# Kernel tuning notes

Measured on AMD Instinct MI355X. Metric: run time of the kernel, lower is better.

## Reference

```python
import jax, jax.numpy as jnp
import numpy as np

B, S, E, H, U = 2048, 64, 512, 512, 512

def setup_inputs() -> dict:
    key = jax.random.key(0)
    ks = jax.random.split(key, 6)
    s = lambda d: 1.0 / np.sqrt(d)
    return {
        "features": jax.random.normal(ks[0], (B, S, E), jnp.float32),
        "hidden": jax.random.normal(ks[1], (B, H), jnp.float32),
        "W1": jax.random.normal(ks[2], (E, U), jnp.float32) * s(E),
        "b1": jnp.zeros((U,), jnp.float32),
        "W2": jax.random.normal(ks[3], (H, U), jnp.float32) * s(H),
        "b2": jnp.zeros((U,), jnp.float32),
        "Wv": jax.random.normal(ks[4], (U, 1), jnp.float32) * s(U),
        "bv": jnp.zeros((1,), jnp.float32),
    }

def reference(features, hidden, W1, b1, W2, b2, Wv, bv):
    # Bahdanau additive attention (dropout at inference = identity).
    h1 = jnp.einsum('bse,eu->bsu', features, W1) + b1          # [B,S,U]
    h2 = hidden @ W2 + b2                                       # [B,U]
    scores = jnp.tanh(h1 + h2[:, None, :]) @ Wv + bv            # [B,S,1]
    weights = jax.nn.softmax(scores, axis=1)                    # softmax over seq
    context = jnp.sum(weights * features, axis=1)               # [B,E]
    return context
```

## Files before the change

kernel.cpp:

```cpp
#include <hip/hip_runtime.h>

typedef _Float16 f16x8 __attribute__((ext_vector_type(8)));
typedef unsigned short u16x4 __attribute__((ext_vector_type(4)));
typedef float f32x4 __attribute__((ext_vector_type(4)));

#define VMWAIT(N) asm volatile("s_waitcnt vmcnt(" #N ")" ::: "memory")
#define LGKM0()   asm volatile("s_waitcnt lgkmcnt(0)" ::: "memory")
#define FENCE()   asm volatile("" ::: "memory")
#define RBAR()    do { FENCE(); __builtin_amdgcn_s_barrier(); FENCE(); } while (0)

__device__ __forceinline__ u16x4 cvt4(float4 v) {
    u16x4 h;
    h[0] = __builtin_bit_cast(unsigned short, (_Float16)v.x);
    h[1] = __builtin_bit_cast(unsigned short, (_Float16)v.y);
    h[2] = __builtin_bit_cast(unsigned short, (_Float16)v.z);
    h[3] = __builtin_bit_cast(unsigned short, (_Float16)v.w);
    return h;
}

__global__ void convert_w_kernel(const float* __restrict__ w1,
                                 const float* __restrict__ w2,
                                 unsigned short* __restrict__ w1img,
                                 unsigned short* __restrict__ w2img) {
    int u = blockIdx.x;
    int k = threadIdx.x + blockIdx.y * 256;
    size_t idx = (size_t)(k >> 5) * 16384 + (size_t)u * 32 + (k & 31);
    _Float16 h1 = (_Float16)w1[(size_t)k * 512 + u];
    _Float16 h2 = (_Float16)w2[(size_t)k * 512 + u];
    w1img[idx] = __builtin_bit_cast(unsigned short, h1);
    w2img[idx] = __builtin_bit_cast(unsigned short, h2);
}

__device__ __forceinline__ void stage_a64(const float* __restrict__ src,
                                          char* As, int tid) {
    const int row = tid >> 2, q = tid & 3;
    const float* p = src + (size_t)row * 512 + q * 4;
    const int sw2 = ((row >> 1) & 3) << 4;
    char* wb = As + row * 64;
    float4 va[4], vb[4];
#define AISS(V, G) { _Pragma("unroll") \
    for (int j_ = 0; j_ < 4; ++j_) V[j_] = *(const float4*)(p + ((G) * 4 + j_) * 16); }
#define APRC(V, G) { _Pragma("unroll") \
    for (int j_ = 0; j_ < 4; ++j_) { \
        const int i_ = (G) * 4 + j_; \
        *(u16x4*)(wb + (i_ >> 1) * 4096 + ((q * 8 + (i_ & 1) * 32) ^ sw2)) = cvt4(V[j_]); } }
    AISS(va, 0); AISS(vb, 1);
    VMWAIT(4); APRC(va, 0); AISS(va, 2);
    VMWAIT(4); APRC(vb, 1); AISS(vb, 3);
    VMWAIT(4); APRC(va, 2); AISS(va, 4);
    VMWAIT(4); APRC(vb, 3); AISS(vb, 5);
    VMWAIT(4); APRC(va, 4); AISS(va, 6);
    VMWAIT(4); APRC(vb, 5); AISS(vb, 7);
    VMWAIT(4); APRC(va, 6);
    VMWAIT(0); APRC(vb, 7);
#undef AISS
#undef APRC
}

__device__ __forceinline__ void chunk_gemm(const char* __restrict__ bcol,
                                           const char* As, const int* aoff,
                                           f32x4 acc[4][4]) {
    f16x8 brA[4], brB[4], afA[4], afB[4];
    #pragma unroll
    for (int i = 0; i < 4; ++i)
        #pragma unroll
        for (int j = 0; j < 4; ++j) acc[i][j] = (f32x4){0.f, 0.f, 0.f, 0.f};
    #pragma unroll
    for (int j = 0; j < 4; ++j) brA[j] = *(const f16x8*)(bcol + j * 1024);
    #pragma unroll
    for (int j = 0; j < 4; ++j) brB[j] = *(const f16x8*)(bcol + 32768 + j * 1024);
    #pragma unroll
    for (int i = 0; i < 4; ++i) afA[i] = *(const f16x8*)(As + aoff[i]);
    #pragma unroll
    for (int tt = 0; tt < 8; ++tt) {
        const int t0 = 2 * tt, t1 = t0 + 1;
        #pragma unroll
        for (int i = 0; i < 4; ++i)
            afB[i] = *(const f16x8*)(As + t1 * 4096 + aoff[i]);
        VMWAIT(4);
        #pragma unroll
        for (int i = 0; i < 4; ++i)
            #pragma unroll
            for (int j = 0; j < 4; ++j)
                acc[i][j] = __builtin_amdgcn_mfma_f32_16x16x32_f16(afA[i], brA[j], acc[i][j], 0, 0, 0);
        if (t0 < 14) {
            #pragma unroll
            for (int j = 0; j < 4; ++j)
                brA[j] = *(const f16x8*)(bcol + (t0 + 2) * 32768 + j * 1024);
        }
        if (t1 < 15) {
            #pragma unroll
            for (int i = 0; i < 4; ++i)
                afA[i] = *(const f16x8*)(As + (t1 + 1) * 4096 + aoff[i]);
        }
        if (t1 < 14) { VMWAIT(4); } else { VMWAIT(0); }
        #pragma unroll
        for (int i = 0; i < 4; ++i)
            #pragma unroll
            for (int j = 0; j < 4; ++j)
                acc[i][j] = __builtin_amdgcn_mfma_f32_16x16x32_f16(afB[i], brB[j], acc[i][j], 0, 0, 0);
        if (t1 < 14) {
            #pragma unroll
            for (int j = 0; j < 4; ++j)
                brB[j] = *(const f16x8*)(bcol + (t1 + 2) * 32768 + j * 1024);
        }
    }
}

__global__ __launch_bounds__(256, 2)
void h2_gemm_kernel(const float* __restrict__ hidden,
                    const char* __restrict__ w2img,
                    const float* __restrict__ b2,
                    float* __restrict__ h2o) {
    __shared__ char As[65536];
    const int tid = threadIdx.x, bm = blockIdx.x, bn = blockIdx.y;
    const int lane = tid & 63, wid = tid >> 6;
    const int lane16 = lane & 15, g = lane >> 4;
    stage_a64(hidden + (size_t)bm * 32768, As, tid);
    __syncthreads();
    int aoff[4];
    #pragma unroll
    for (int i = 0; i < 4; ++i)
        aoff[i] = (i * 16 + lane16) * 64 + ((g ^ ((lane16 >> 1) & 3)) << 4);
    const char* bcol = w2img + (size_t)(bn * 256 + wid * 64 + lane16) * 64 + g * 16;
    f32x4 acc[4][4];
    chunk_gemm(bcol, As, aoff, acc);
    #pragma unroll
    for (int j = 0; j < 4; ++j) {
        int col = bn * 256 + wid * 64 + j * 16 + lane16;
        float bb = b2[col];
        #pragma unroll
        for (int i = 0; i < 4; ++i)
            #pragma unroll
            for (int r = 0; r < 4; ++r)
                h2o[(size_t)(bm * 64 + i * 16 + g * 4 + r) * 512 + col] = acc[i][j][r] + bb;
    }
}

__device__ __forceinline__ void chunk64_lowreg(const char* __restrict__ bcol,
                                               const char* As, const int* aoff,
                                               f32x4 acc[4][4]) {
    f16x8 brE[4], brO[4];
    #pragma unroll
    for (int i = 0; i < 4; ++i)
        #pragma unroll
        for (int j = 0; j < 4; ++j) acc[i][j] = (f32x4){0.f, 0.f, 0.f, 0.f};
    #pragma unroll
    for (int j = 0; j < 4; ++j) brE[j] = *(const f16x8*)(bcol + j * 1024);
    #pragma unroll
    for (int j = 0; j < 4; ++j) brO[j] = *(const f16x8*)(bcol + 32768 + j * 1024);
    #pragma unroll
    for (int t = 0; t < 16; ++t) {
        f16x8 af[4];
        #pragma unroll
        for (int i = 0; i < 4; ++i)
            af[i] = *(const f16x8*)(As + t * 4096 + aoff[i]);
        if (t < 14) { VMWAIT(4); } else { VMWAIT(0); }
        LGKM0();
        if ((t & 1) == 0) {
            #pragma unroll
            for (int i = 0; i < 4; ++i)
                #pragma unroll
                for (int j = 0; j < 4; ++j)
                    acc[i][j] = __builtin_amdgcn_mfma_f32_16x16x32_f16(af[i], brE[j], acc[i][j], 0, 0, 0);
            FENCE();
            if (t < 14) {
                #pragma unroll
                for (int j = 0; j < 4; ++j)
                    brE[j] = *(const f16x8*)(bcol + (t + 2) * 32768 + j * 1024);
            }
        } else {
            #pragma unroll
            for (int i = 0; i < 4; ++i)
                #pragma unroll
                for (int j = 0; j < 4; ++j)
                    acc[i][j] = __builtin_amdgcn_mfma_f32_16x16x32_f16(af[i], brO[j], acc[i][j], 0, 0, 0);
            FENCE();
            if (t < 14) {
                #pragma unroll
                for (int j = 0; j < 4; ++j)
                    brO[j] = *(const f16x8*)(bcol + (t + 2) * 32768 + j * 1024);
            }
        }
        FENCE();
    }
}

__global__ __launch_bounds__(512, 4)
void fused_all_kernel(const float* __restrict__ feat,
                      const char* __restrict__ w1img,
                      const float* __restrict__ h2,
                      const float* __restrict__ b1,
                      const float* __restrict__ wv,
                      float* __restrict__ out) {
    __shared__ char As[65536];
    __shared__ float hhs[512];
    __shared__ float wvs[512];
    __shared__ float spl[512];
    __shared__ float wsm[64];
    __shared__ float cpart[512];

    const int tid = threadIdx.x;
    const int bm = (blockIdx.x & 7) * 256 + (blockIdx.x >> 3);
    const int lane16 = tid & 15, g = (tid >> 4) & 3;
    const int wid = tid >> 6;

    {
        const int row = tid >> 3, q = tid & 7;
        const float* p = feat + (size_t)bm * 32768 + (size_t)row * 512 + q * 4;
        char* wb = As + row * 64 + (((q >> 1) ^ ((row >> 1) & 3)) << 4) + (q & 1) * 8;
        float hb = b1[tid];
        float hv = h2[(size_t)bm * 512 + tid];
        float wv_ = wv[tid];
        FENCE();
        float4 v[16];
        #pragma unroll
        for (int j = 0; j < 16; ++j) v[j] = *(const float4*)(p + j * 32);
        FENCE();
        VMWAIT(16);
        hhs[tid] = hb + hv;
        wvs[tid] = wv_;
        VMWAIT(12);
        #pragma unroll
        for (int j = 0; j < 4; ++j)  *(u16x4*)(wb + j * 4096) = cvt4(v[j]);
        VMWAIT(8);
        #pragma unroll
        for (int j = 4; j < 8; ++j)  *(u16x4*)(wb + j * 4096) = cvt4(v[j]);
        VMWAIT(4);
        #pragma unroll
        for (int j = 8; j < 12; ++j) *(u16x4*)(wb + j * 4096) = cvt4(v[j]);
        VMWAIT(0);
        #pragma unroll
        for (int j = 12; j < 16; ++j) *(u16x4*)(wb + j * 4096) = cvt4(v[j]);
    }
    LGKM0();
    RBAR();

    int aoff[4];
    #pragma unroll
    for (int i = 0; i < 4; ++i)
        aoff[i] = (i * 16 + lane16) * 64 + ((g ^ ((lane16 >> 1) & 3)) << 4);
    const char* bcol = w1img + (size_t)(wid * 64 + lane16) * 64 + g * 16;
    f32x4 acc[4][4];
    chunk64_lowreg(bcol, As, aoff, acc);

    float hhv[4], wvv[4];
    #pragma unroll
    for (int j = 0; j < 4; ++j) {
        int col = wid * 64 + j * 16 + lane16;
        hhv[j] = hhs[col];
        wvv[j] = wvs[col];
    }

    #pragma unroll
    for (int i = 0; i < 4; ++i)
        #pragma unroll
        for (int r = 0; r < 4; ++r) {
            float s = 0.f;
            #pragma unroll
            for (int j = 0; j < 4; ++j) {
                float h = acc[i][j][r] + hhv[j];
                float ex = __expf(2.f * h);
                s += (1.f - 2.f * __builtin_amdgcn_rcpf(ex + 1.f)) * wvv[j];
            }
            s += __shfl_xor(s, 1); s += __shfl_xor(s, 2);
            s += __shfl_xor(s, 4); s += __shfl_xor(s, 8);
            if (lane16 == 0) spl[(i * 16 + g * 4 + r) * 8 + wid] = s;
        }
    LGKM0();
    RBAR();

    if (tid < 64) {
        float s = ((spl[tid * 8 + 0] + spl[tid * 8 + 1]) + (spl[tid * 8 + 2] + spl[tid * 8 + 3])) +
                  ((spl[tid * 8 + 4] + spl[tid * 8 + 5]) + (spl[tid * 8 + 6] + spl[tid * 8 + 7]));
        float m = s;
        #pragma unroll
        for (int off = 32; off; off >>= 1) m = fmaxf(m, __shfl_xor(m, off));
        float e = __expf(s - m);
        float sum = e;
        #pragma unroll
        for (int off = 32; off; off >>= 1) sum += __shfl_xor(sum, off);
        wsm[tid] = e / sum;
        LGKM0();
    }
    RBAR();

    {
        const int t2 = tid & 255, half = tid >> 8;
        const int kst = t2 >> 4;
        const int base = kst * 4096 + (t2 & 3) * 4;
        const int ksl = (t2 >> 2) & 3;
        float ax = 0.f, ay = 0.f;
        #pragma unroll 8
        for (int si = 0; si < 32; ++si) {
            const int s = half * 32 + ((si + kst) & 31);
            unsigned vv = *(const unsigned*)(As + base + s * 64 +
                                             ((ksl ^ ((s >> 1) & 3)) << 4));
            float w = wsm[s];
            ax += w * (float)__builtin_bit_cast(_Float16, (unsigned short)(vv & 0xffffu));
            ay += w * (float)__builtin_bit_cast(_Float16, (unsigned short)(vv >> 16));
        }
        if (half == 1) { cpart[t2 * 2] = ax; cpart[t2 * 2 + 1] = ay; }
        LGKM0();
        RBAR();
        if (half == 0) {
            ax += cpart[t2 * 2]; ay += cpart[t2 * 2 + 1];
            ((float2*)out)[(size_t)bm * 256 + t2] = make_float2(ax, ay);
        }
    }
}

extern "C" void kernel_launch(void* const* d_in, const int* in_sizes, int n_in,
                              void* d_out, int out_size, void* d_ws, size_t ws_size,
                              hipStream_t stream) {
    (void)in_sizes; (void)n_in; (void)out_size; (void)ws_size;
    const float* feat   = (const float*)d_in[0];
    const float* hidden = (const float*)d_in[1];
    const float* W1     = (const float*)d_in[2];
    const float* b1     = (const float*)d_in[3];
    const float* W2     = (const float*)d_in[4];
    const float* b2     = (const float*)d_in[5];
    const float* Wv     = (const float*)d_in[6];
    float* out = (float*)d_out;

    char* ws = (char*)d_ws;
    unsigned short* w1img = (unsigned short*)(ws);
    unsigned short* w2img = (unsigned short*)(ws + 524288);
    float* h2 = (float*)(ws + 1048576);

    convert_w_kernel<<<dim3(512, 2), dim3(256), 0, stream>>>(W1, W2, w1img, w2img);
    h2_gemm_kernel<<<dim3(32, 2), dim3(256), 0, stream>>>(hidden, (const char*)w2img, b2, h2);
    fused_all_kernel<<<dim3(2048), dim3(512), 0, stream>>>(feat, (const char*)w1img, h2, b1, Wv, out);
}
```

Before: 139.5 us.

## Warp-specialize fused attention kernel with producer waves prefetching next batch

The fused kernel becomes a persistent 1024-thread block that handles 8 batch rows. Waves 0-7 act as consumers and run the GEMM, tanh/softmax and context reduction. Waves 8-15 act as producers: they load and convert the next batch's features into a second LDS buffer while the consumers work on the current one. The aim is to hide global feature-load latency behind MFMA compute. In exchange, grid size drops to 256 blocks, LDS use doubles to about 130KB per block, and occupancy falls to one block per CU, which may leave CUs underfilled (256 blocks against 256 CUs).

```diff
diff --git a/kernel.cpp b/kernel.cpp
--- a/kernel.cpp
+++ b/kernel.cpp
@@ -145,6 +145,8 @@
     for (int i = 0; i < 4; ++i)
         #pragma unroll
         for (int j = 0; j < 4; ++j) acc[i][j] = (f32x4){0.f, 0.f, 0.f, 0.f};
+    VMWAIT(0);
+    FENCE();
     #pragma unroll
     for (int j = 0; j < 4; ++j) brE[j] = *(const f16x8*)(bcol + j * 1024);
     #pragma unroll
@@ -186,52 +188,55 @@
     }
 }
 
-__global__ __launch_bounds__(512, 4)
+__global__ __launch_bounds__(1024, 4)
 void fused_all_kernel(const float* __restrict__ feat,
                       const char* __restrict__ w1img,
                       const float* __restrict__ h2,
                       const float* __restrict__ b1,
                       const float* __restrict__ wv,
                       float* __restrict__ out) {
-    __shared__ char As[65536];
-    __shared__ float hhs[512];
+    __shared__ char As[2][65536];
+    __shared__ float hhs[2][512];
     __shared__ float wvs[512];
     __shared__ float spl[512];
     __shared__ float wsm[64];
     __shared__ float cpart[512];
 
     const int tid = threadIdx.x;
-    const int bm = (blockIdx.x & 7) * 256 + (blockIdx.x >> 3);
+    const bool consumer = (tid < 512);
+    const int blk = (blockIdx.x & 7) * 32 + (blockIdx.x >> 3);
+    const int b0 = blk * 8;
     const int lane16 = tid & 15, g = (tid >> 4) & 3;
     const int wid = tid >> 6;
 
+    const int pid = tid & 511;
+    const int prow = pid >> 3, pq = pid & 7;
+    const int pswz = (((pq >> 1) ^ ((prow >> 1) & 3)) << 4) + (pq & 1) * 8;
+
+    float b1v = b1[pid];
+    float wvv0 = 0.f, h2v0 = 0.f;
+    if (consumer) {
+        h2v0 = h2[(size_t)b0 * 512 + tid];
+        wvv0 = wv[tid];
+    }
+    FENCE();
     {
-        const int row = tid >> 3, q = tid & 7;
-        const float* p = feat + (size_t)bm * 32768 + (size_t)row * 512 + q * 4;
-        char* wb = As + row * 64 + (((q >> 1) ^ ((row >> 1) & 3)) << 4) + (q & 1) * 8;
-        float hb = b1[tid];
-        float hv = h2[(size_t)bm * 512 + tid];
-        float wv_ = wv[tid];
+        const int r0 = tid >> 4, sub = tid & 15, q8 = sub >> 1, koff = (sub & 1) * 8;
+        const float* p0 = feat + (size_t)b0 * 32768 + (size_t)r0 * 512 + q8 * 4;
+        char* wb0 = As[0] + r0 * 64 + (((q8 >> 1) ^ ((r0 >> 1) & 3)) << 4) + (q8 & 1) * 8;
+        float4 v[8];
+        #pragma unroll
+        for (int j = 0; j < 8; ++j) v[j] = *(const float4*)(p0 + (koff + j) * 32);
         FENCE();
-        float4 v[16];
-        #pragma unroll
-        for (int j = 0; j < 16; ++j) v[j] = *(const float4*)(p + j * 32);
-        FENCE();
-        VMWAIT(16);
-        hhs[tid] = hb + hv;
-        wvs[tid] = wv_;
-        VMWAIT(12);
-        #pragma unroll
-        for (int j = 0; j < 4; ++j)  *(u16x4*)(wb + j * 4096) = cvt4(v[j]);
-        VMWAIT(8);
-        #pragma unroll
-        for (int j = 4; j < 8; ++j)  *(u16x4*)(wb + j * 4096) = cvt4(v[j]);
         VMWAIT(4);
-        #pragma unroll
-        for (int j = 8; j < 12; ++j) *(u16x4*)(wb + j * 4096) = cvt4(v[j]);
+        if (consumer) { wvs[tid] = wvv0; hhs[0][tid] = b1v + h2v0; }
+        #pragma unroll
+        for (int j = 0; j < 4; ++j)
+            *(u16x4*)(wb0 + (koff + j) * 4096) = cvt4(v[j]);
         VMWAIT(0);
         #pragma unroll
-        for (int j = 12; j < 16; ++j) *(u16x4*)(wb + j * 4096) = cvt4(v[j]);
+        for (int j = 4; j < 8; ++j)
+            *(u16x4*)(wb0 + (koff + j) * 4096) = cvt4(v[j]);
     }
     LGKM0();
     RBAR();
@@ -241,71 +246,97 @@
     for (int i = 0; i < 4; ++i)
         aoff[i] = (i * 16 + lane16) * 64 + ((g ^ ((lane16 >> 1) & 3)) << 4);
     const char* bcol = w1img + (size_t)(wid * 64 + lane16) * 64 + g * 16;
-    f32x4 acc[4][4];
-    chunk64_lowreg(bcol, As, aoff, acc);
-
-    float hhv[4], wvv[4];
-    #pragma unroll
-    for (int j = 0; j < 4; ++j) {
-        int col = wid * 64 + j * 16 + lane16;
-        hhv[j] = hhs[col];
-        wvv[j] = wvs[col];
-    }
-
-    #pragma unroll
-    for (int i = 0; i < 4; ++i)
-        #pragma unroll
-        for (int r = 0; r < 4; ++r) {
-            float s = 0.f;
+
+    #pragma unroll 1
+    for (int it = 0; it < 8; ++it) {
+        const int cur = it & 1;
+        float4 pv[16];
+        float h2n = 0.f;
+        float ax = 0.f, ay = 0.f;
+
+        if (consumer) {
+            f32x4 acc[4][4];
+            chunk64_lowreg(bcol, As[cur], aoff, acc);
+            float hhv[4], wvv[4];
             #pragma unroll
             for (int j = 0; j < 4; ++j) {
-                float h = acc[i][j][r] + hhv[j];
-                float ex = __expf(2.f * h);
-                s += (1.f - 2.f * __builtin_amdgcn_rcpf(ex + 1.f)) * wvv[j];
+                int col = wid * 64 + j * 16 + lane16;
+                hhv[j] = hhs[cur][col];
+                wvv[j] = wvs[col];
             }
-            s += __shfl_xor(s, 1); s += __shfl_xor(s, 2);
-            s += __shfl_xor(s, 4); s += __shfl_xor(s, 8);
-            if (lane16 == 0) spl[(i * 16 + g * 4 + r) * 8 + wid] = s;
-        }
-    LGKM0();
-    RBAR();
-
-    if (tid < 64) {
-        float s = ((spl[tid * 8 + 0] + spl[tid * 8 + 1]) + (spl[tid * 8 + 2] + spl[tid * 8 + 3])) +
-                  ((spl[tid * 8 + 4] + spl[tid * 8 + 5]) + (spl[tid * 8 + 6] + spl[tid * 8 + 7]));
-        float m = s;
-        #pragma unroll
-        for (int off = 32; off; off >>= 1) m = fmaxf(m, __shfl_xor(m, off));
-        float e = __expf(s - m);
-        float sum = e;
-        #pragma unroll
-        for (int off = 32; off; off >>= 1) sum += __shfl_xor(sum, off);
-        wsm[tid] = e / sum;
-        LGKM0();
-    }
-    RBAR();
-
-    {
-        const int t2 = tid & 255, half = tid >> 8;
-        const int kst = t2 >> 4;
-        const int base = kst * 4096 + (t2 & 3) * 4;
-        const int ksl = (t2 >> 2) & 3;
-        float ax = 0.f, ay = 0.f;
-        #pragma unroll 8
-        for (int si = 0; si < 32; ++si) {
-            const int s = half * 32 + ((si + kst) & 31);
-            unsigned vv = *(const unsigned*)(As + base + s * 64 +
-                                             ((ksl ^ ((s >> 1) & 3)) << 4));
-            float w = wsm[s];
-            ax += w * (float)__builtin_bit_cast(_Float16, (unsigned short)(vv & 0xffffu));
-            ay += w * (float)__builtin_bit_cast(_Float16, (unsigned short)(vv >> 16));
-        }
-        if (half == 1) { cpart[t2 * 2] = ax; cpart[t2 * 2 + 1] = ay; }
-        LGKM0();
+            #pragma unroll
+            for (int i = 0; i < 4; ++i)
+                #pragma unroll
+                for (int r = 0; r < 4; ++r) {
+                    float s = 0.f;
+                    #pragma unroll
+                    for (int j = 0; j < 4; ++j) {
+                        float h = acc[i][j][r] + hhv[j];
+                        float ex = __expf(2.f * h);
+                        s += (1.f - 2.f * __builtin_amdgcn_rcpf(ex + 1.f)) * wvv[j];
+                    }
+                    s += __shfl_xor(s, 1); s += __shfl_xor(s, 2);
+                    s += __shfl_xor(s, 4); s += __shfl_xor(s, 8);
+                    if (lane16 == 0) spl[(i * 16 + g * 4 + r) * 8 + wid] = s;
+                }
+            LGKM0();
+        } else if (it < 7) {
+            const float* pn = feat + (size_t)(b0 + it + 1) * 32768 +
+                              (size_t)prow * 512 + pq * 4;
+            #pragma unroll
+            for (int j = 0; j < 16; ++j) pv[j] = *(const float4*)(pn + j * 32);
+            h2n = h2[(size_t)(b0 + it + 1) * 512 + pid];
+            FENCE();
+        }
         RBAR();
-        if (half == 0) {
+
+        if (tid < 64) {
+            float s = ((spl[tid * 8 + 0] + spl[tid * 8 + 1]) + (spl[tid * 8 + 2] + spl[tid * 8 + 3])) +
+                      ((spl[tid * 8 + 4] + spl[tid * 8 + 5]) + (spl[tid * 8 + 6] + spl[tid * 8 + 7]));
+            float m = s;
+            #pragma unroll
+            for (int off = 32; off; off >>= 1) m = fmaxf(m, __shfl_xor(m, off));
+            float e = __expf(s - m);
+            float sum = e;
+            #pragma unroll
+            for (int off = 32; off; off >>= 1) sum += __shfl_xor(sum, off);
+            wsm[tid] = e / sum;
+            LGKM0();
+        }
+        RBAR();
+
+        if (consumer) {
+            const int t2 = tid & 255, half = tid >> 8;
+            const int kst = t2 >> 4;
+            const int base = kst * 4096 + (t2 & 3) * 4;
+            const int ksl = (t2 >> 2) & 3;
+            #pragma unroll 8
+            for (int si = 0; si < 32; ++si) {
+                const int s = half * 32 + ((si + kst) & 31);
+                unsigned vv = *(const unsigned*)(As[cur] + base + s * 64 +
+                                                 ((ksl ^ ((s >> 1) & 3)) << 4));
+                float w = wsm[s];
+                ax += w * (float)__builtin_bit_cast(_Float16, (unsigned short)(vv & 0xffffu));
+                ay += w * (float)__builtin_bit_cast(_Float16, (unsigned short)(vv >> 16));
+            }
+            if (half == 1) { cpart[t2 * 2] = ax; cpart[t2 * 2 + 1] = ay; }
+            LGKM0();
+        } else if (it < 7) {
+            VMWAIT(0);
+            FENCE();
+            char* pwb = As[cur ^ 1] + prow * 64 + pswz;
+            #pragma unroll
+            for (int j = 0; j < 16; ++j)
+                *(u16x4*)(pwb + j * 4096) = cvt4(pv[j]);
+            hhs[cur ^ 1][pid] = b1v + h2n;
+            LGKM0();
+        }
+        RBAR();
+
+        if (consumer && (tid >> 8) == 0) {
+            const int t2 = tid & 255;
             ax += cpart[t2 * 2]; ay += cpart[t2 * 2 + 1];
-            ((float2*)out)[(size_t)bm * 256 + t2] = make_float2(ax, ay);
+            ((float2*)out)[(size_t)(b0 + it) * 256 + t2] = make_float2(ax, ay);
         }
     }
 }
@@ -330,5 +361,5 @@
 
     convert_w_kernel<<<dim3(512, 2), dim3(256), 0, stream>>>(W1, W2, w1img, w2img);
     h2_gemm_kernel<<<dim3(32, 2), dim3(256), 0, stream>>>(hidden, (const char*)w2img, b2, h2);
-    fused_all_kernel<<<dim3(2048), dim3(512), 0, stream>>>(feat, (const char*)w1img, h2, b1, Wv, out);
-}
+    fused_all_kernel<<<dim3(256), dim3(1024), 0, stream>>>(feat, (const char*)w1img, h2, b1, Wv, out);
+}
```

Measured after the change: 437.6 us. +213.7%, slower.
